# Kernel tuning notes

Hardware: AMD Instinct MI355X
Metric: run time of the kernel (lower is better)

The kernel has to match this reference:

```python
import jax, jax.numpy as jnp
import numpy as np

EPS = 1e-5
K_NN = 16

def _lin1d(x, W, b):
    # 1x1 Conv1d: x (B,C,N) -> (B,O,N)
    return jnp.einsum('oc,bcn->bon', W, x) + b[None, :, None]

def _lin2d(x, W, b):
    # 1x1 Conv2d: x (B,C,N,K) -> (B,O,N,K)
    return jnp.einsum('oc,bcnk->bonk', W, x) + b[None, :, None, None]

def _bn2d(x, gamma, beta):
    # train-mode BatchNorm2d over (B, N, K) per channel
    mean = jnp.mean(x, axis=(0, 2, 3), keepdims=True)
    var = jnp.var(x, axis=(0, 2, 3), keepdims=True)
    xh = (x - mean) * jax.lax.rsqrt(var + EPS)
    return gamma[None, :, None, None] * xh + beta[None, :, None, None]

def _knn_idx(pq, ps, k):
    # pq (B,3,N), ps (B,3,M) -> idx (B,N,K) of k nearest support points
    d2 = (jnp.sum(pq * pq, axis=1)[:, :, None]
          + jnp.sum(ps * ps, axis=1)[:, None, :]
          - 2.0 * jnp.einsum('bcn,bcm->bnm', pq, ps))
    _, idx = jax.lax.top_k(-d2, k)
    return idx

def _group(x, idx):
    # x (B,C,M), idx (B,N,K) -> (B,C,N,K)
    return jnp.take_along_axis(x[:, :, None, :], idx[:, None, :, :], axis=3)

def setup_inputs() -> dict:
    key = jax.random.key(0)
    ks = jax.random.split(key, 20)
    B, C, D, N, M, H = 4, 128, 64, 2048, 2048, 256
    s = lambda k, shape, scale: (jax.random.normal(k, shape, dtype=jnp.float32) * scale)
    return {
        'pq': s(ks[0], (B, 3, N), 1.0),
        'fq': s(ks[1], (B, C, N), 1.0),
        'ps': s(ks[2], (B, 3, M), 1.0),
        'fs': s(ks[3], (B, C, M), 1.0),
        'Wq': s(ks[4], (D, C), 0.05), 'bq': jnp.zeros((D,), jnp.float32),
        'Wk': s(ks[5], (D, C), 0.05), 'bk': jnp.zeros((D,), jnp.float32),
        'Wv': s(ks[6], (D, C), 0.05), 'bv': jnp.zeros((D,), jnp.float32),
        'Wp1': s(ks[7], (D, 3), 0.2), 'bp1': jnp.zeros((D,), jnp.float32),
        'gp': jnp.ones((D,), jnp.float32), 'btp': jnp.zeros((D,), jnp.float32),
        'Wp2': s(ks[8], (D, D), 0.05), 'bp2': jnp.zeros((D,), jnp.float32),
        'Wa1': s(ks[9], (H, D), 0.05), 'ba1': jnp.zeros((H,), jnp.float32),
        'ga': jnp.ones((H,), jnp.float32), 'bta': jnp.zeros((H,), jnp.float32),
        'Wa2': s(ks[10], (D, H), 0.05), 'ba2': jnp.zeros((D,), jnp.float32),
        'We': s(ks[11], (C, D), 0.05), 'be': jnp.zeros((C,), jnp.float32),
    }

def reference(pq, fq, ps, fs, Wq, bq, Wk, bk, Wv, bv,
              Wp1, bp1, gp, btp, Wp2, bp2,
              Wa1, ba1, ga, bta, Wa2, ba2, We, be):
    identity = fq
    q = _lin1d(fq, Wq, bq)          # (B,D,N)
    k = _lin1d(fs, Wk, bk)          # (B,D,M)
    v = _lin1d(fs, Wv, bv)          # (B,D,M)
    idx = _knn_idx(pq, ps, K_NN)    # (B,N,K)
    key_g = _group(k, idx)          # (B,D,N,K)
    qk_rel = q[:, :, :, None] - key_g
    pos_rel = pq[:, :, :, None] - _group(ps, idx)  # (B,3,N,K)
    # pos_mlp: conv-bn-relu-conv
    pe = _lin2d(pos_rel, Wp1, bp1)
    pe = jax.nn.relu(_bn2d(pe, gp, btp))
    pe = _lin2d(pe, Wp2, bp2)       # (B,D,N,K)
    # attn_mlp: conv-bn-relu-conv
    a = _lin2d(qk_rel + pe, Wa1, ba1)
    a = jax.nn.relu(_bn2d(a, ga, bta))
    a = _lin2d(a, Wa2, ba2)         # (B,D,N,K)
    attn = jax.nn.softmax(a, axis=-1)
    val = _group(v, idx) + pe       # (B,D,N,K)
    agg = jnp.einsum('bcnk,bcnk->bcn', attn, val)
    return _lin1d(agg, We, be) + identity
```

## Files before the change

kernel.cpp:

```cpp
#include <hip/hip_runtime.h>
#include <stdint.h>

#define NN 2048
#define MM 2048
#define NSAMP 131072

typedef float  fv4 __attribute__((ext_vector_type(4)));
typedef short  bfv8 __attribute__((ext_vector_type(8)));
typedef short  bfv4 __attribute__((ext_vector_type(4)));
typedef unsigned short u16;
typedef unsigned long long u64;

__device__ inline u16 f2bf(float x){
  unsigned u = __float_as_uint(x);
  return (u16)((u + 0x7FFFu + ((u>>16)&1u)) >> 16);
}
__device__ inline float bf2f(u16 u){ return __uint_as_float(((unsigned)u)<<16); }
#define MFMA16 __builtin_amdgcn_mfma_f32_16x16x32_bf16

__global__ __launch_bounds__(256) void k_front(
    const float* __restrict__ pq, const float* __restrict__ ps,
    const float* __restrict__ fq, const float* __restrict__ fs,
    const float* __restrict__ Wq, const float* __restrict__ Wk, const float* __restrict__ Wv,
    const float* __restrict__ Wp2, const float* __restrict__ Wa2, const float* __restrict__ We,
    const float* __restrict__ bq, const float* __restrict__ bk, const float* __restrict__ bv,
    u16* __restrict__ Wp2bf, u16* __restrict__ Wa2bf, u16* __restrict__ Webf,
    float* __restrict__ qT, float* __restrict__ kT, float* __restrict__ vT,
    int* __restrict__ idxb, float* __restrict__ posPart) {
  __shared__ __align__(16) unsigned char smem[35072];
  const int bid = blockIdx.x;
  const int t = threadIdx.x;

  if (bid < 64) {
    int gid = bid * 256 + t;
    if (gid < 4096)  Wp2bf[gid] = f2bf(Wp2[gid]);
    if (gid < 16384) Wa2bf[gid] = f2bf(Wa2[gid]);
    if (gid < 8192)  Webf[gid]  = f2bf(We[gid]);
    return;
  }

  if (bid < 320) {
    u16* tile0 = (u16*)smem;
    u16* tile1 = (u16*)(smem + 8704);
    int r = bid - 64;
    int b = r >> 6, p0 = (r & 63) * 32;
    int w = t >> 6, l = t & 63, lq = l >> 4, ln = l & 15;
    {
      int cq = t >> 3, n4 = (t & 7) * 4;
      #pragma unroll
      for (int it = 0; it < 4; ++it) {
        int c = it * 32 + cq;
        fv4 vq = *(const fv4*)&fq[(b*128 + c)*2048 + p0 + n4];
        fv4 vs = *(const fv4*)&fs[(b*128 + c)*2048 + p0 + n4];
        #pragma unroll
        for (int j = 0; j < 4; ++j) {
          tile0[(n4 + j)*136 + c] = f2bf(vq[j]);
          tile1[(n4 + j)*136 + c] = f2bf(vs[j]);
        }
      }
    }
    bfv8 A[3][4];
    #pragma unroll
    for (int mat = 0; mat < 3; ++mat) {
      const float* Wf = mat == 0 ? Wq : (mat == 1 ? Wk : Wv);
      #pragma unroll
      for (int kk = 0; kk < 4; ++kk) {
        const float* src = Wf + (w*16 + ln)*128 + kk*32 + lq*8;
        fv4 a0 = *(const fv4*)src, a1 = *(const fv4*)(src + 4);
        u16 tmp[8];
        #pragma unroll
        for (int e = 0; e < 4; ++e) { tmp[e] = f2bf(a0[e]); tmp[4+e] = f2bf(a1[e]); }
        A[mat][kk] = *(const bfv8*)tmp;
      }
    }
    __syncthreads();
    fv4 acc[3][2];
    #pragma unroll
    for (int mat = 0; mat < 3; ++mat) {
      const u16* tl = mat == 0 ? tile0 : tile1;
      #pragma unroll
      for (int nt = 0; nt < 2; ++nt) {
        fv4 a = {0.f,0.f,0.f,0.f};
        #pragma unroll
        for (int kk = 0; kk < 4; ++kk) {
          bfv8 bb = *(const bfv8*)&tl[(nt*16 + ln)*136 + kk*32 + lq*8];
          a = MFMA16(A[mat][kk], bb, a, 0, 0, 0);
        }
        acc[mat][nt] = a;
      }
    }
    #pragma unroll
    for (int mat = 0; mat < 3; ++mat) {
      float* dst = mat == 0 ? qT : (mat == 1 ? kT : vT);
      const float* bia = mat == 0 ? bq : (mat == 1 ? bk : bv);
      fv4 bq4 = *(const fv4*)&bia[w*16 + lq*4];
      #pragma unroll
      for (int nt = 0; nt < 2; ++nt) {
        fv4 o = acc[mat][nt] + bq4;
        *(fv4*)&dst[(b*NN + p0 + nt*16 + ln)*64 + w*16 + lq*4] = o;
      }
    }
    return;
  }

  {
    u64*   cand = (u64*)smem;
    float* sacc = (float*)(smem + 34816);
    int w = t >> 6, lane = t & 63;
    int blk = bid - 320;
    int qi = blk * 4 + w;
    int b = qi >> 11, n = qi & 2047;
    const float* pqb = pq + b * 3 * NN;
    const float* psb = ps + b * 3 * MM;
    float qx = pqb[n], qy = pqb[NN + n], qz = pqb[2 * NN + n];
    float qq = qx * qx + qy * qy + qz * qz;

    u64 A[16], Bv[16];
    #pragma unroll
    for (int j = 0; j < 16; ++j) {
      int m = lane + 64 * j;
      float sx = psb[m], sy = psb[MM + m], sz = psb[2 * MM + m];
      float ss  = sx * sx + sy * sy + sz * sz;
      float d2 = qq + ss - 2.f * (qx * sx + qy * sy + qz * sz);
      unsigned bu = __float_as_uint(d2);
      bu = (bu & 0x80000000u) ? ~bu : (bu | 0x80000000u);
      A[j] = (((u64)bu) << 32) | (unsigned)m;
    }
    #pragma unroll
    for (int j = 0; j < 16; ++j) {
      int m = lane + 64 * (j + 16);
      float sx = psb[m], sy = psb[MM + m], sz = psb[2 * MM + m];
      float ss  = sx * sx + sy * sy + sz * sz;
      float d2 = qq + ss - 2.f * (qx * sx + qy * sy + qz * sz);
      unsigned bu = __float_as_uint(d2);
      bu = (bu & 0x80000000u) ? ~bu : (bu | 0x80000000u);
      Bv[j] = (((u64)bu) << 32) | (unsigned)m;
    }
    #pragma unroll
    for (int k = 2; k <= 16; k <<= 1) {
      #pragma unroll
      for (int j = k >> 1; j > 0; j >>= 1) {
        #pragma unroll
        for (int i = 0; i < 16; ++i) {
          int l2 = i ^ j;
          if (l2 > i) {
            bool up = ((i & k) == 0);
            { u64 x = A[i], y = A[l2];
              bool sw = up ? (y < x) : (x < y);
              A[i] = sw ? y : x;  A[l2] = sw ? x : y; }
            { u64 x = Bv[i], y = Bv[l2];
              bool sw = up ? (y < x) : (x < y);
              Bv[i] = sw ? y : x; Bv[l2] = sw ? x : y; }
          }
        }
      }
    }
    #pragma unroll
    for (int i = 0; i < 16; ++i) {
      u64 y = Bv[15 - i];
      A[i] = A[i] < y ? A[i] : y;
    }
    #pragma unroll
    for (int j = 8; j > 0; j >>= 1) {
      #pragma unroll
      for (int i = 0; i < 16; ++i) {
        int l2 = i ^ j;
        if (l2 > i) {
          u64 x = A[i], y = A[l2];
          bool sw = (y < x);
          A[i] = sw ? y : x;  A[l2] = sw ? x : y;
        }
      }
    }
    #pragma unroll
    for (int i = 0; i < 16; ++i) cand[w*1088 + lane*17 + i] = A[i];
    float s0=0.f,s1=0.f,s2=0.f,s3=0.f,s4=0.f,s5=0.f,s6=0.f,s7=0.f,s8=0.f;
    int head = 0;
    for (int r = 0; r < 16; ++r) {
      u64 v = (head < 16) ? cand[w*1088 + lane*17 + head] : ~0ULL;
      u64 mv = v;
      #pragma unroll
      for (int off = 32; off > 0; off >>= 1) {
        u64 o = __shfl_xor(mv, off, 64);
        mv = o < mv ? o : mv;
      }
      if (v == mv) head++;
      unsigned m = (unsigned)(mv & 0xFFFFFFFFu);
      if (lane == 0) idxb[qi * 16 + r] = (int)m;
      float r0 = qx - psb[m], r1 = qy - psb[MM + m], r2 = qz - psb[2*MM + m];
      s0 += r0; s1 += r1; s2 += r2;
      s3 += r0*r0; s4 += r0*r1; s5 += r0*r2;
      s6 += r1*r1; s7 += r1*r2; s8 += r2*r2;
    }
    if (lane == 0) {
      sacc[w*9+0]=s0; sacc[w*9+1]=s1; sacc[w*9+2]=s2; sacc[w*9+3]=s3; sacc[w*9+4]=s4;
      sacc[w*9+5]=s5; sacc[w*9+6]=s6; sacc[w*9+7]=s7; sacc[w*9+8]=s8;
    }
    __syncthreads();
    if (t < 9) posPart[blk * 12 + t] =
        sacc[t] + sacc[9 + t] + sacc[18 + t] + sacc[27 + t];
  }
}

__global__ __launch_bounds__(256) void k_posfinal(
    const float* __restrict__ Wp1, const float* __restrict__ bp1,
    const float* __restrict__ gp, const float* __restrict__ btp,
    const float* __restrict__ posPart, float* __restrict__ Wp1f, float* __restrict__ bp1f) {
  __shared__ float red[4][9];
  __shared__ float st[9];
  int t = threadIdx.x;
  int w = t >> 6, lane = t & 63;
  float s[9];
  #pragma unroll
  for (int i = 0; i < 9; ++i) s[i] = 0.f;
  #pragma unroll
  for (int it = 0; it < 8; ++it) {
    const float* p = posPart + (it * 256 + t) * 12;
    fv4 a = *(const fv4*)p;
    fv4 b4 = *(const fv4*)(p + 4);
    float c8 = p[8];
    s[0]+=a.x; s[1]+=a.y; s[2]+=a.z; s[3]+=a.w;
    s[4]+=b4.x; s[5]+=b4.y; s[6]+=b4.z; s[7]+=b4.w;
    s[8]+=c8;
  }
  #pragma unroll
  for (int off = 32; off > 0; off >>= 1)
    #pragma unroll
    for (int i = 0; i < 9; ++i) s[i] += __shfl_xor(s[i], off, 64);
  if (lane == 0)
    #pragma unroll
    for (int i = 0; i < 9; ++i) red[w][i] = s[i];
  __syncthreads();
  if (t < 9) st[t] = red[0][t] + red[1][t] + red[2][t] + red[3][t];
  __syncthreads();
  if (t < 64) {
    int d = t;
    const float invN = 1.f / (float)NSAMP;
    float m0 = st[0]*invN, m1 = st[1]*invN, m2 = st[2]*invN;
    float C00 = st[3]*invN - m0*m0, C01 = st[4]*invN - m0*m1, C02 = st[5]*invN - m0*m2;
    float C11 = st[6]*invN - m1*m1, C12 = st[7]*invN - m1*m2, C22 = st[8]*invN - m2*m2;
    float w0 = Wp1[d*3], w1 = Wp1[d*3+1], w2 = Wp1[d*3+2];
    float mean = w0*m0 + w1*m1 + w2*m2 + bp1[d];
    float var = w0*w0*C00 + w1*w1*C11 + w2*w2*C22 + 2.f*(w0*w1*C01 + w0*w2*C02 + w1*w2*C12);
    float scale = gp[d] * rsqrtf(var + 1e-5f);
    Wp1f[d*3]   = scale * w0;
    Wp1f[d*3+1] = scale * w1;
    Wp1f[d*3+2] = scale * w2;
    bp1f[d] = btp[d] + scale * (bp1[d] - mean);
  }
}

__global__ __launch_bounds__(256) void k_ystats(
    const float* __restrict__ pq, const float* __restrict__ ps,
    const float* __restrict__ qT, const float* __restrict__ kT,
    const int* __restrict__ idxb,
    const float* __restrict__ Wp1f, const float* __restrict__ bp1f,
    const u16* __restrict__ Wp2bf, const float* __restrict__ bp2,
    float* __restrict__ Gpart, float* __restrict__ ySumPart) {
  __shared__ __align__(16) unsigned char smem[21760];
  u16*   hp   = (u16*)smem;
  u16*   y2   = (u16*)(smem + 9216);
  float* r3   = (float*)(smem + 18432);
  float* qc   = (float*)(smem + 19200);
  int*   idxA = (int*)(smem + 20224);
  float* sWp1 = (float*)(smem + 20480);
  float* sbp1 = (float*)(smem + 21248);
  float* sbp2 = (float*)(smem + 21504);

  const int t = threadIdx.x;
  const int w = t >> 6, l = t & 63, lq = l >> 4, ln = l & 15;
  const int d0 = 16*w + lq*4;

  if (t < 192) sWp1[t] = Wp1f[t];
  if (t < 64){ sbp1[t] = bp1f[t]; sbp2[t] = bp2[t]; }

  bfv8 Ape[2];
  #pragma unroll
  for (int kk = 0; kk < 2; ++kk)
    Ape[kk] = *(const bfv8*)(Wp2bf + (16*w + ln)*64 + kk*32 + lq*8);

  fv4 gacc[4];
  #pragma unroll
  for (int nt = 0; nt < 4; ++nt) gacc[nt] = (fv4){0.f,0.f,0.f,0.f};
  float ys[4] = {0.f, 0.f, 0.f, 0.f};
  __syncthreads();

  for (int ch = 0; ch < 4; ++ch) {
    const int p0 = blockIdx.x * 16 + ch * 4;
    const int b  = p0 >> 11;
    const int bN = b * 2048;
    if (t < 64) idxA[t] = idxb[p0*16 + t];
    qc[t] = qT[(p0 + (t>>6))*64 + (t & 63)];
    __syncthreads();
    if (t < 192) { int c = t >> 6, s = t & 63; int n = (p0 + (s>>4)) & 2047;
      r3[c*64 + s] = pq[(b*3+c)*NN + n] - ps[(b*3+c)*MM + idxA[s]]; }
    __syncthreads();
    { int s = t >> 2, iq = t & 3;
      float r0 = r3[s], r1 = r3[64+s], r2 = r3[128+s];
      u16 tmp[16];
      #pragma unroll
      for (int e = 0; e < 16; ++e) { int i = iq*16 + e;
        float v = sbp1[i] + sWp1[i*3]*r0 + sWp1[i*3+1]*r1 + sWp1[i*3+2]*r2;
        tmp[e] = f2bf(fmaxf(v, 0.f)); }
      *(bfv8*)&hp[s*72 + iq*16]     = *(const bfv8*)&tmp[0];
      *(bfv8*)&hp[s*72 + iq*16 + 8] = *(const bfv8*)&tmp[8];
    }
    __syncthreads();
    {
      fv4 pe[4];
      #pragma unroll
      for (int nt = 0; nt < 4; ++nt) {
        fv4 acc = {0.f,0.f,0.f,0.f};
        #pragma unroll
        for (int kk = 0; kk < 2; ++kk) {
          bfv8 bb = *(const bfv8*)&hp[(nt*16 + ln)*72 + kk*32 + lq*8];
          acc = MFMA16(Ape[kk], bb, acc, 0, 0, 0);
        }
        pe[nt] = acc;
      }
      fv4 bp2q = *(const fv4*)&sbp2[d0];
      #pragma unroll
      for (int nt = 0; nt < 4; ++nt) {
        int s = nt*16 + ln;
        int mi = idxA[s];
        fv4 kg = *(const fv4*)(kT + (bN + mi)*64 + d0);
        fv4 qv = *(const fv4*)&qc[nt*64 + d0];
        fv4 yv = qv - kg + pe[nt] + bp2q;
        #pragma unroll
        for (int r = 0; r < 4; ++r) { y2[(d0 + r)*72 + s] = f2bf(yv[r]); ys[r] += yv[r]; }
      }
    }
    __syncthreads();
    #pragma unroll
    for (int kk = 0; kk < 2; ++kk) {
      bfv8 aa = *(const bfv8*)&y2[(16*w + ln)*72 + kk*32 + lq*8];
      #pragma unroll
      for (int nt = 0; nt < 4; ++nt) {
        bfv8 bb = *(const bfv8*)&y2[(nt*16 + ln)*72 + kk*32 + lq*8];
        gacc[nt] = MFMA16(aa, bb, gacc[nt], 0, 0, 0);
      }
    }
    __syncthreads();
  }
  #pragma unroll
  for (int nt = 0; nt < 4; ++nt)
    #pragma unroll
    for (int r = 0; r < 4; ++r)
      Gpart[blockIdx.x*4096 + (16*w + lq*4 + r)*64 + nt*16 + ln] = gacc[nt][r];
  #pragma unroll
  for (int off = 1; off <= 8; off <<= 1) {
    #pragma unroll
    for (int r = 0; r < 4; ++r) ys[r] += __shfl_xor(ys[r], off, 64);
  }
  if (ln == 0) {
    #pragma unroll
    for (int r = 0; r < 4; ++r) ySumPart[blockIdx.x*64 + d0 + r] = ys[r];
  }
}

__global__ __launch_bounds__(256) void k_gred(
    const float* __restrict__ Gpart, const float* __restrict__ ySumPart,
    float* __restrict__ G, float* __restrict__ ySum) {
  int bid = blockIdx.x, t = threadIdx.x;
  if (bid < 16) {
    int j = bid*256 + t;
    float s = 0.f;
    for (int p = 0; p < 512; ++p) s += Gpart[p*4096 + j];
    G[j] = s;
  } else if (t < 64) {
    float s = 0.f;
    for (int p = 0; p < 512; ++p) s += ySumPart[p*64 + t];
    ySum[t] = s;
  }
}

__global__ __launch_bounds__(256) void k_attnfinal(
    const float* __restrict__ Wa1, const float* __restrict__ ba1,
    const float* __restrict__ ga, const float* __restrict__ bta,
    const float* __restrict__ ySum, const float* __restrict__ G,
    u16* __restrict__ Wa1fbf, float* __restrict__ ba1f) {
  __shared__ float red[256];
  __shared__ float mu[64];
  __shared__ float sc[1];
  int h = blockIdx.x, t = threadIdx.x;
  const float invN = 1.f / (float)NSAMP;
  if (t < 64) mu[t] = ySum[t] * invN;
  __syncthreads();
  float acc = 0.f;
  #pragma unroll
  for (int e = 0; e < 16; ++e) {
    int pi = t*16 + e, i = pi >> 6, j = pi & 63;
    float cov = G[pi]*invN - mu[i]*mu[j];
    acc += Wa1[h*64 + i] * Wa1[h*64 + j] * cov;
  }
  red[t] = acc;
  __syncthreads();
  for (int s = 128; s > 0; s >>= 1) { if (t < s) red[t] += red[t + s]; __syncthreads(); }
  float var = red[0];
  __syncthreads();
  red[t] = (t < 64) ? Wa1[h*64 + t] * mu[t] : 0.f;
  __syncthreads();
  for (int s = 128; s > 0; s >>= 1) { if (t < s) red[t] += red[t + s]; __syncthreads(); }
  if (t == 0) {
    float mean  = red[0] + ba1[h];
    float scale = ga[h] * rsqrtf(var + 1e-5f);
    sc[0] = scale;
    ba1f[h] = bta[h] + scale * (ba1[h] - mean);
  }
  __syncthreads();
  if (t < 64) Wa1fbf[h*64 + t] = f2bf(sc[0] * Wa1[h*64 + t]);
}

__global__ __launch_bounds__(256) void k_main(
    const float* __restrict__ pq, const float* __restrict__ ps,
    const float* __restrict__ qT, const float* __restrict__ kT, const float* __restrict__ vT,
    const int* __restrict__ idxb,
    const float* __restrict__ Wp1f, const float* __restrict__ bp1f,
    const u16* __restrict__ Wp2bf, const float* __restrict__ bp2,
    const u16* __restrict__ Wa1fbf, const float* __restrict__ ba1f,
    const u16* __restrict__ Wa2bf, const float* __restrict__ ba2,
    const u16* __restrict__ Webf, const float* __restrict__ be,
    const float* __restrict__ fq,
    u16* __restrict__ aggbf, float* __restrict__ out) {
  __shared__ __align__(16) unsigned char smem[65024];
  u16*   hp   = (u16*)smem;
  u16*   ha   = (u16*)smem;
  u16*   ylds = (u16*)(smem + 33792);
  float* at   = (float*)(smem + 33792);
  u16*   vt   = (u16*)(smem + 51200);
  float* r3   = (float*)(smem + 60416);
  float* qc   = (float*)(smem + 61184);
  int*   idxA = (int*)(smem + 62208);
  float* sWp1 = (float*)(smem + 62464);
  float* sbp1 = (float*)(smem + 63232);
  float* sbp2 = (float*)(smem + 63488);
  float* sba1 = (float*)(smem + 63744);
  float* sba2 = (float*)(smem + 64768);

  const int t = threadIdx.x;
  const int w = t >> 6, l = t & 63, lq = l >> 4, ln = l & 15;
  const int d0 = 16*w + lq*4;

  if (t < 192) sWp1[t] = Wp1f[t];
  if (t < 64){ sbp1[t] = bp1f[t]; sbp2[t] = bp2[t]; sba2[t] = ba2[t]; }
  sba1[t] = ba1f[t];

  bfv8 Ape[2], A1[4][2], A2[8];
  #pragma unroll
  for (int kk = 0; kk < 2; ++kk)
    Ape[kk] = *(const bfv8*)(Wp2bf + (16*w + ln)*64 + kk*32 + lq*8);
  #pragma unroll
  for (int mt = 0; mt < 4; ++mt)
    #pragma unroll
    for (int kk = 0; kk < 2; ++kk)
      A1[mt][kk] = *(const bfv8*)(Wa1fbf + (64*w + mt*16 + ln)*64 + kk*32 + lq*8);
  #pragma unroll
  for (int kk = 0; kk < 8; ++kk)
    A2[kk] = *(const bfv8*)(Wa2bf + (16*w + ln)*256 + kk*32 + lq*8);
  __syncthreads();

  for (int ch = 0; ch < 4; ++ch) {
    const int p0 = blockIdx.x * 16 + ch * 4;
    const int b  = p0 >> 11;
    const int bN = b * 2048;
    if (t < 64) idxA[t] = idxb[p0*16 + t];
    qc[t] = qT[(p0 + (t>>6))*64 + (t & 63)];
    __syncthreads();
    if (t < 192) { int c = t >> 6, s = t & 63; int n = (p0 + (s>>4)) & 2047;
      r3[c*64 + s] = pq[(b*3+c)*NN + n] - ps[(b*3+c)*MM + idxA[s]]; }
    __syncthreads();
    { int s = t >> 2, iq = t & 3;
      float r0 = r3[s], r1 = r3[64+s], r2 = r3[128+s];
      u16 tmp[16];
      #pragma unroll
      for (int e = 0; e < 16; ++e) { int i = iq*16 + e;
        float v = sbp1[i] + sWp1[i*3]*r0 + sWp1[i*3+1]*r1 + sWp1[i*3+2]*r2;
        tmp[e] = f2bf(fmaxf(v, 0.f)); }
      *(bfv8*)&hp[s*72 + iq*16]     = *(const bfv8*)&tmp[0];
      *(bfv8*)&hp[s*72 + iq*16 + 8] = *(const bfv8*)&tmp[8];
    }
    __syncthreads();
    {
      fv4 pe[4];
      #pragma unroll
      for (int nt = 0; nt < 4; ++nt) {
        fv4 acc = {0.f,0.f,0.f,0.f};
        #pragma unroll
        for (int kk = 0; kk < 2; ++kk) {
          bfv8 bb = *(const bfv8*)&hp[(nt*16 + ln)*72 + kk*32 + lq*8];
          acc = MFMA16(Ape[kk], bb, acc, 0, 0, 0);
        }
        pe[nt] = acc;
      }
      fv4 bp2q = *(const fv4*)&sbp2[d0];
      #pragma unroll
      for (int nt = 0; nt < 4; ++nt) {
        int s = nt*16 + ln;
        int mi = idxA[s];
        fv4 kg = *(const fv4*)(kT + (bN + mi)*64 + d0);
        fv4 vg = *(const fv4*)(vT + (bN + mi)*64 + d0);
        fv4 qv = *(const fv4*)&qc[nt*64 + d0];
        fv4 pv = pe[nt] + bp2q;
        fv4 yv = qv - kg + pv;
        fv4 vv = vg + pv;
        u16 yp[4], vp[4];
        #pragma unroll
        for (int r = 0; r < 4; ++r) { yp[r] = f2bf(yv[r]); vp[r] = f2bf(vv[r]); }
        *(bfv4*)&ylds[s*72 + d0] = *(const bfv4*)yp;
        *(bfv4*)&vt[s*72 + d0]   = *(const bfv4*)vp;
      }
    }
    __syncthreads();
    #pragma unroll
    for (int nt = 0; nt < 4; ++nt) {
      int s = nt*16 + ln;
      bfv8 b0 = *(const bfv8*)&ylds[s*72 + lq*8];
      bfv8 b1 = *(const bfv8*)&ylds[s*72 + 32 + lq*8];
      #pragma unroll
      for (int mt = 0; mt < 4; ++mt) {
        fv4 acc = {0.f,0.f,0.f,0.f};
        acc = MFMA16(A1[mt][0], b0, acc, 0, 0, 0);
        acc = MFMA16(A1[mt][1], b1, acc, 0, 0, 0);
        int h0 = 64*w + mt*16 + lq*4;
        fv4 bq = *(const fv4*)&sba1[h0];
        u16 hv[4];
        #pragma unroll
        for (int r = 0; r < 4; ++r) hv[r] = f2bf(fmaxf(acc[r] + bq[r], 0.f));
        *(bfv4*)&ha[s*264 + h0] = *(const bfv4*)hv;
      }
    }
    __syncthreads();
    {
      fv4 acc2[4];
      #pragma unroll
      for (int nt = 0; nt < 4; ++nt) acc2[nt] = (fv4){0.f,0.f,0.f,0.f};
      #pragma unroll
      for (int kk = 0; kk < 8; ++kk) {
        #pragma unroll
        for (int nt = 0; nt < 4; ++nt) {
          bfv8 bb = *(const bfv8*)&ha[(nt*16 + ln)*264 + kk*32 + lq*8];
          acc2[nt] = MFMA16(A2[kk], bb, acc2[nt], 0, 0, 0);
        }
      }
      fv4 ba2q = *(const fv4*)&sba2[d0];
      #pragma unroll
      for (int nt = 0; nt < 4; ++nt) {
        int s = nt*16 + ln;
        fv4 o = acc2[nt] + ba2q;
        *(fv4*)&at[s*68 + d0] = o;
      }
    }
    __syncthreads();
    {
      int dd = t & 63, pt = t >> 6;
      float a[16];
      #pragma unroll
      for (int k = 0; k < 16; ++k) a[k] = at[(pt*16 + k)*68 + dd];
      float mx = a[0];
      #pragma unroll
      for (int k = 1; k < 16; ++k) mx = fmaxf(mx, a[k]);
      float sum = 0.f, num = 0.f;
      #pragma unroll
      for (int k = 0; k < 16; ++k) {
        float e = __expf(a[k] - mx);
        sum += e;
        num += e * bf2f(vt[(pt*16 + k)*72 + dd]);
      }
      aggbf[(p0 + pt)*64 + dd] = f2bf(num / sum);
    }
    __syncthreads();
  }
  {
    const int P0 = blockIdx.x * 16;
    const int b  = P0 >> 11;
    const int n0 = P0 & 2047;
    bfv8 EA[2][2];
    #pragma unroll
    for (int mt = 0; mt < 2; ++mt)
      #pragma unroll
      for (int kk = 0; kk < 2; ++kk)
        EA[mt][kk] = *(const bfv8*)(Webf + ((w*2 + mt)*16 + ln)*64 + kk*32 + lq*8);
    const u16* bp = aggbf + (P0 + ln)*64;
    bfv8 b0 = *(const bfv8*)(bp + lq*8);
    bfv8 b1 = *(const bfv8*)(bp + 32 + lq*8);
    fv4 eacc[2];
    #pragma unroll
    for (int mt = 0; mt < 2; ++mt) {
      fv4 a = {0.f,0.f,0.f,0.f};
      a = MFMA16(EA[mt][0], b0, a, 0, 0, 0);
      a = MFMA16(EA[mt][1], b1, a, 0, 0, 0);
      eacc[mt] = a;
    }
    #pragma unroll
    for (int mt = 0; mt < 2; ++mt) {
      int c0 = (w*2 + mt)*16 + lq*4;
      fv4 bev = *(const fv4*)&be[c0];
      #pragma unroll
      for (int r = 0; r < 4; ++r) {
        int c = c0 + r;
        int o = (b*128 + c)*2048 + n0 + ln;
        out[o] = eacc[mt][r] + bev[r] + fq[o];
      }
    }
  }
}

extern "C" void kernel_launch(void* const* d_in, const int* in_sizes, int n_in,
                              void* d_out, int out_size, void* d_ws, size_t ws_size,
                              hipStream_t stream) {
  (void)in_sizes; (void)n_in; (void)out_size; (void)ws_size;
  const float* pq  = (const float*)d_in[0];
  const float* fq  = (const float*)d_in[1];
  const float* ps  = (const float*)d_in[2];
  const float* fs  = (const float*)d_in[3];
  const float* Wq  = (const float*)d_in[4];  const float* bq  = (const float*)d_in[5];
  const float* Wk  = (const float*)d_in[6];  const float* bk  = (const float*)d_in[7];
  const float* Wv  = (const float*)d_in[8];  const float* bv  = (const float*)d_in[9];
  const float* Wp1 = (const float*)d_in[10]; const float* bp1 = (const float*)d_in[11];
  const float* gp  = (const float*)d_in[12]; const float* btp = (const float*)d_in[13];
  const float* Wp2 = (const float*)d_in[14]; const float* bp2 = (const float*)d_in[15];
  const float* Wa1 = (const float*)d_in[16]; const float* ba1 = (const float*)d_in[17];
  const float* ga  = (const float*)d_in[18]; const float* bta = (const float*)d_in[19];
  const float* Wa2 = (const float*)d_in[20]; const float* ba2 = (const float*)d_in[21];
  const float* We  = (const float*)d_in[22]; const float* be  = (const float*)d_in[23];
  float* ws = (float*)d_ws;
  float* qT    = ws;
  float* kT    = ws + 524288;
  float* vT    = ws + 1048576;
  u16*   aggbf = (u16*)(ws + 1572864);
  int*   idxb  = (int*)(ws + 2097152);
  float* Wp1f  = ws + 2375680;
  float* bp1f  = ws + 2375872;
  float* ba1f  = ws + 2375936;
  float* G     = ws + 2376192;
  float* ySum  = ws + 2380288;
  float* ySumP = ws + 2380352;
  u16*   Wp2bf  = (u16*)(ws + 2413120);
  u16*   Wa2bf  = (u16*)(ws + 2415168);
  u16*   Wa1fbf = (u16*)(ws + 2423360);
  u16*   Webf   = (u16*)(ws + 2431552);
  float* posPart = ws + 2435648;
  float* Gpart   = ws + 2460224;
  float* out   = (float*)d_out;

  k_front<<<2368, 256, 0, stream>>>(pq, ps, fq, fs, Wq, Wk, Wv, Wp2, Wa2, We,
                                    bq, bk, bv, Wp2bf, Wa2bf, Webf,
                                    qT, kT, vT, idxb, posPart);
  k_posfinal<<<1, 256, 0, stream>>>(Wp1, bp1, gp, btp, posPart, Wp1f, bp1f);
  k_ystats<<<512, 256, 0, stream>>>(pq, ps, qT, kT, idxb, Wp1f, bp1f, Wp2bf, bp2,
                                    Gpart, ySumP);
  k_gred<<<17, 256, 0, stream>>>(Gpart, ySumP, G, ySum);
  k_attnfinal<<<256, 256, 0, stream>>>(Wa1, ba1, ga, bta, ySum, G, Wa1fbf, ba1f);
  k_main<<<512, 256, 0, stream>>>(pq, ps, qT, kT, vT, idxb, Wp1f, bp1f, Wp2bf, bp2,
                                  Wa1fbf, ba1f, Wa2bf, ba2, Webf, be, fq, aggbf, out);
}
```

Before: 246.6 us.

## Fuse pos-BN finalize into ystats, halve per-block points, shuffle softmax in main

```diff
diff --git a/kernel.cpp b/kernel.cpp
--- a/kernel.cpp
+++ b/kernel.cpp
@@ -202,62 +202,17 @@
   }
 }
 
-__global__ __launch_bounds__(256) void k_posfinal(
-    const float* __restrict__ Wp1, const float* __restrict__ bp1,
-    const float* __restrict__ gp, const float* __restrict__ btp,
-    const float* __restrict__ posPart, float* __restrict__ Wp1f, float* __restrict__ bp1f) {
-  __shared__ float red[4][9];
-  __shared__ float st[9];
-  int t = threadIdx.x;
-  int w = t >> 6, lane = t & 63;
-  float s[9];
-  #pragma unroll
-  for (int i = 0; i < 9; ++i) s[i] = 0.f;
-  #pragma unroll
-  for (int it = 0; it < 8; ++it) {
-    const float* p = posPart + (it * 256 + t) * 12;
-    fv4 a = *(const fv4*)p;
-    fv4 b4 = *(const fv4*)(p + 4);
-    float c8 = p[8];
-    s[0]+=a.x; s[1]+=a.y; s[2]+=a.z; s[3]+=a.w;
-    s[4]+=b4.x; s[5]+=b4.y; s[6]+=b4.z; s[7]+=b4.w;
-    s[8]+=c8;
-  }
-  #pragma unroll
-  for (int off = 32; off > 0; off >>= 1)
-    #pragma unroll
-    for (int i = 0; i < 9; ++i) s[i] += __shfl_xor(s[i], off, 64);
-  if (lane == 0)
-    #pragma unroll
-    for (int i = 0; i < 9; ++i) red[w][i] = s[i];
-  __syncthreads();
-  if (t < 9) st[t] = red[0][t] + red[1][t] + red[2][t] + red[3][t];
-  __syncthreads();
-  if (t < 64) {
-    int d = t;
-    const float invN = 1.f / (float)NSAMP;
-    float m0 = st[0]*invN, m1 = st[1]*invN, m2 = st[2]*invN;
-    float C00 = st[3]*invN - m0*m0, C01 = st[4]*invN - m0*m1, C02 = st[5]*invN - m0*m2;
-    float C11 = st[6]*invN - m1*m1, C12 = st[7]*invN - m1*m2, C22 = st[8]*invN - m2*m2;
-    float w0 = Wp1[d*3], w1 = Wp1[d*3+1], w2 = Wp1[d*3+2];
-    float mean = w0*m0 + w1*m1 + w2*m2 + bp1[d];
-    float var = w0*w0*C00 + w1*w1*C11 + w2*w2*C22 + 2.f*(w0*w1*C01 + w0*w2*C02 + w1*w2*C12);
-    float scale = gp[d] * rsqrtf(var + 1e-5f);
-    Wp1f[d*3]   = scale * w0;
-    Wp1f[d*3+1] = scale * w1;
-    Wp1f[d*3+2] = scale * w2;
-    bp1f[d] = btp[d] + scale * (bp1[d] - mean);
-  }
-}
-
 __global__ __launch_bounds__(256) void k_ystats(
     const float* __restrict__ pq, const float* __restrict__ ps,
     const float* __restrict__ qT, const float* __restrict__ kT,
     const int* __restrict__ idxb,
-    const float* __restrict__ Wp1f, const float* __restrict__ bp1f,
+    const float* __restrict__ Wp1, const float* __restrict__ bp1,
+    const float* __restrict__ gp, const float* __restrict__ btp,
+    const float* __restrict__ posPart,
     const u16* __restrict__ Wp2bf, const float* __restrict__ bp2,
-    float* __restrict__ Gpart, float* __restrict__ ySumPart) {
-  __shared__ __align__(16) unsigned char smem[21760];
+    u16* __restrict__ Gpart16, float* __restrict__ ySumPart,
+    float* __restrict__ Wp1fG, float* __restrict__ bp1fG) {
+  __shared__ __align__(16) unsigned char smem[22144];
   u16*   hp   = (u16*)smem;
   u16*   y2   = (u16*)(smem + 9216);
   float* r3   = (float*)(smem + 18432);
@@ -266,14 +221,59 @@
   float* sWp1 = (float*)(smem + 20480);
   float* sbp1 = (float*)(smem + 21248);
   float* sbp2 = (float*)(smem + 21504);
+  float* redp = (float*)(smem + 21760);
 
   const int t = threadIdx.x;
   const int w = t >> 6, l = t & 63, lq = l >> 4, ln = l & 15;
   const int d0 = 16*w + lq*4;
 
-  if (t < 192) sWp1[t] = Wp1f[t];
-  if (t < 64){ sbp1[t] = bp1f[t]; sbp2[t] = bp2[t]; }
-
+  {
+    float s[9];
+    #pragma unroll
+    for (int i = 0; i < 9; ++i) s[i] = 0.f;
+    #pragma unroll
+    for (int it = 0; it < 8; ++it) {
+      const float* p = posPart + (it * 256 + t) * 12;
+      fv4 a = *(const fv4*)p;
+      fv4 b4 = *(const fv4*)(p + 4);
+      float c8 = p[8];
+      s[0]+=a.x; s[1]+=a.y; s[2]+=a.z; s[3]+=a.w;
+      s[4]+=b4.x; s[5]+=b4.y; s[6]+=b4.z; s[7]+=b4.w;
+      s[8]+=c8;
+    }
+    #pragma unroll
+    for (int off = 32; off > 0; off >>= 1)
+      #pragma unroll
+      for (int i = 0; i < 9; ++i) s[i] += __shfl_xor(s[i], off, 64);
+    if (l == 0)
+      #pragma unroll
+      for (int i = 0; i < 9; ++i) redp[w*9 + i] = s[i];
+    __syncthreads();
+    if (t < 9) redp[36 + t] = redp[t] + redp[9+t] + redp[18+t] + redp[27+t];
+    __syncthreads();
+    if (t < 64) {
+      const float* st = redp + 36;
+      int d = t;
+      const float invN = 1.f / (float)NSAMP;
+      float m0 = st[0]*invN, m1 = st[1]*invN, m2 = st[2]*invN;
+      float C00 = st[3]*invN - m0*m0, C01 = st[4]*invN - m0*m1, C02 = st[5]*invN - m0*m2;
+      float C11 = st[6]*invN - m1*m1, C12 = st[7]*invN - m1*m2, C22 = st[8]*invN - m2*m2;
+      float w0 = Wp1[d*3], w1 = Wp1[d*3+1], w2 = Wp1[d*3+2];
+      float mean = w0*m0 + w1*m1 + w2*m2 + bp1[d];
+      float var = w0*w0*C00 + w1*w1*C11 + w2*w2*C22 + 2.f*(w0*w1*C01 + w0*w2*C02 + w1*w2*C12);
+      float scale = gp[d] * rsqrtf(var + 1e-5f);
+      sWp1[d*3]   = scale * w0;
+      sWp1[d*3+1] = scale * w1;
+      sWp1[d*3+2] = scale * w2;
+      float bf = btp[d] + scale * (bp1[d] - mean);
+      sbp1[d] = bf;
+      sbp2[d] = bp2[d];
+      if (blockIdx.x == 0) {
+        Wp1fG[d*3] = sWp1[d*3]; Wp1fG[d*3+1] = sWp1[d*3+1]; Wp1fG[d*3+2] = sWp1[d*3+2];
+        bp1fG[d] = bf;
+      }
+    }
+  }
   bfv8 Ape[2];
   #pragma unroll
   for (int kk = 0; kk < 2; ++kk)
@@ -285,8 +285,8 @@
   float ys[4] = {0.f, 0.f, 0.f, 0.f};
   __syncthreads();
 
-  for (int ch = 0; ch < 4; ++ch) {
-    const int p0 = blockIdx.x * 16 + ch * 4;
+  for (int ch = 0; ch < 2; ++ch) {
+    const int p0 = blockIdx.x * 8 + ch * 4;
     const int b  = p0 >> 11;
     const int bN = b * 2048;
     if (t < 64) idxA[t] = idxb[p0*16 + t];
@@ -346,7 +346,7 @@
   for (int nt = 0; nt < 4; ++nt)
     #pragma unroll
     for (int r = 0; r < 4; ++r)
-      Gpart[blockIdx.x*4096 + (16*w + lq*4 + r)*64 + nt*16 + ln] = gacc[nt][r];
+      Gpart16[blockIdx.x*4096 + (16*w + lq*4 + r)*64 + nt*16 + ln] = f2bf(gacc[nt][r]);
   #pragma unroll
   for (int off = 1; off <= 8; off <<= 1) {
     #pragma unroll
@@ -359,18 +359,29 @@
 }
 
 __global__ __launch_bounds__(256) void k_gred(
-    const float* __restrict__ Gpart, const float* __restrict__ ySumPart,
+    const u16* __restrict__ Gpart16, const float* __restrict__ ySumPart,
     float* __restrict__ G, float* __restrict__ ySum) {
+  __shared__ float red[256];
   int bid = blockIdx.x, t = threadIdx.x;
-  if (bid < 16) {
-    int j = bid*256 + t;
+  if (bid < 256) {
+    int j0 = bid * 16, tj = t & 15, st = t >> 4;
     float s = 0.f;
-    for (int p = 0; p < 512; ++p) s += Gpart[p*4096 + j];
-    G[j] = s;
-  } else if (t < 64) {
-    float s = 0.f;
-    for (int p = 0; p < 512; ++p) s += ySumPart[p*64 + t];
-    ySum[t] = s;
+    for (int p = 0; p < 64; ++p)
+      s += bf2f(Gpart16[(st*64 + p)*4096 + j0 + tj]);
+    red[t] = s;
+    __syncthreads();
+    if (t < 16) {
+      float ss = 0.f;
+      #pragma unroll
+      for (int k = 0; k < 16; ++k) ss += red[k*16 + t];
+      G[j0 + t] = ss;
+    }
+  } else {
+    if (t < 64) {
+      float s = 0.f;
+      for (int p = 0; p < 1024; ++p) s += ySumPart[p*64 + t];
+      ySum[t] = s;
+    }
   }
 }
 
@@ -411,7 +422,7 @@
   if (t < 64) Wa1fbf[h*64 + t] = f2bf(sc[0] * Wa1[h*64 + t]);
 }
 
-__global__ __launch_bounds__(256) void k_main(
+__global__ __launch_bounds__(256, 3) void k_main(
     const float* __restrict__ pq, const float* __restrict__ ps,
     const float* __restrict__ qT, const float* __restrict__ kT, const float* __restrict__ vT,
     const int* __restrict__ idxb,
@@ -420,22 +431,20 @@
     const u16* __restrict__ Wa1fbf, const float* __restrict__ ba1f,
     const u16* __restrict__ Wa2bf, const float* __restrict__ ba2,
     const u16* __restrict__ Webf, const float* __restrict__ be,
-    const float* __restrict__ fq,
-    u16* __restrict__ aggbf, float* __restrict__ out) {
-  __shared__ __align__(16) unsigned char smem[65024];
+    const float* __restrict__ fq, float* __restrict__ out) {
+  __shared__ __align__(16) unsigned char smem[48896];
   u16*   hp   = (u16*)smem;
   u16*   ha   = (u16*)smem;
   u16*   ylds = (u16*)(smem + 33792);
-  float* at   = (float*)(smem + 33792);
-  u16*   vt   = (u16*)(smem + 51200);
-  float* r3   = (float*)(smem + 60416);
-  float* qc   = (float*)(smem + 61184);
-  int*   idxA = (int*)(smem + 62208);
-  float* sWp1 = (float*)(smem + 62464);
-  float* sbp1 = (float*)(smem + 63232);
-  float* sbp2 = (float*)(smem + 63488);
-  float* sba1 = (float*)(smem + 63744);
-  float* sba2 = (float*)(smem + 64768);
+  u16*   agg  = (u16*)(smem + 43008);
+  float* r3   = (float*)(smem + 44288);
+  float* qc   = (float*)(smem + 45056);
+  int*   idxA = (int*)(smem + 46080);
+  float* sWp1 = (float*)(smem + 46336);
+  float* sbp1 = (float*)(smem + 47104);
+  float* sbp2 = (float*)(smem + 47360);
+  float* sba1 = (float*)(smem + 47616);
+  float* sba2 = (float*)(smem + 48640);
 
   const int t = threadIdx.x;
   const int w = t >> 6, l = t & 63, lq = l >> 4, ln = l & 15;
@@ -459,8 +468,8 @@
     A2[kk] = *(const bfv8*)(Wa2bf + (16*w + ln)*256 + kk*32 + lq*8);
   __syncthreads();
 
-  for (int ch = 0; ch < 4; ++ch) {
-    const int p0 = blockIdx.x * 16 + ch * 4;
+  for (int ch = 0; ch < 2; ++ch) {
+    const int p0 = blockIdx.x * 8 + ch * 4;
     const int b  = p0 >> 11;
     const int bN = b * 2048;
     if (t < 64) idxA[t] = idxb[p0*16 + t];
@@ -480,6 +489,7 @@
       *(bfv8*)&hp[s*72 + iq*16 + 8] = *(const bfv8*)&tmp[8];
     }
     __syncthreads();
+    fv4 vvr[4];
     {
       fv4 pe[4];
       #pragma unroll
@@ -502,12 +512,11 @@
         fv4 qv = *(const fv4*)&qc[nt*64 + d0];
         fv4 pv = pe[nt] + bp2q;
         fv4 yv = qv - kg + pv;
-        fv4 vv = vg + pv;
-        u16 yp[4], vp[4];
-        #pragma unroll
-        for (int r = 0; r < 4; ++r) { yp[r] = f2bf(yv[r]); vp[r] = f2bf(vv[r]); }
+        vvr[nt] = vg + pv;
+        u16 yp[4];
+        #pragma unroll
+        for (int r = 0; r < 4; ++r) yp[r] = f2bf(yv[r]);
         *(bfv4*)&ylds[s*72 + d0] = *(const bfv4*)yp;
-        *(bfv4*)&vt[s*72 + d0]   = *(const bfv4*)vp;
       }
     }
     __syncthreads();
@@ -545,33 +554,31 @@
       fv4 ba2q = *(const fv4*)&sba2[d0];
       #pragma unroll
       for (int nt = 0; nt < 4; ++nt) {
-        int s = nt*16 + ln;
-        fv4 o = acc2[nt] + ba2q;
-        *(fv4*)&at[s*68 + d0] = o;
-      }
-    }
-    __syncthreads();
-    {
-      int dd = t & 63, pt = t >> 6;
-      float a[16];
-      #pragma unroll
-      for (int k = 0; k < 16; ++k) a[k] = at[(pt*16 + k)*68 + dd];
-      float mx = a[0];
-      #pragma unroll
-      for (int k = 1; k < 16; ++k) mx = fmaxf(mx, a[k]);
-      float sum = 0.f, num = 0.f;
-      #pragma unroll
-      for (int k = 0; k < 16; ++k) {
-        float e = __expf(a[k] - mx);
-        sum += e;
-        num += e * bf2f(vt[(pt*16 + k)*72 + dd]);
-      }
-      aggbf[(p0 + pt)*64 + dd] = f2bf(num / sum);
+        fv4 a4 = acc2[nt] + ba2q;
+        u16 o4[4];
+        #pragma unroll
+        for (int r = 0; r < 4; ++r) {
+          float m = a4[r];
+          m = fmaxf(m, __shfl_xor(m, 1, 64));
+          m = fmaxf(m, __shfl_xor(m, 2, 64));
+          m = fmaxf(m, __shfl_xor(m, 4, 64));
+          m = fmaxf(m, __shfl_xor(m, 8, 64));
+          float e = __expf(a4[r] - m);
+          float se = e;
+          se += __shfl_xor(se, 1, 64); se += __shfl_xor(se, 2, 64);
+          se += __shfl_xor(se, 4, 64); se += __shfl_xor(se, 8, 64);
+          float nu = e * vvr[nt][r];
+          nu += __shfl_xor(nu, 1, 64); nu += __shfl_xor(nu, 2, 64);
+          nu += __shfl_xor(nu, 4, 64); nu += __shfl_xor(nu, 8, 64);
+          o4[r] = f2bf(nu / se);
+        }
+        if (ln == 0) *(bfv4*)&agg[(ch*4 + nt)*72 + d0] = *(const bfv4*)o4;
+      }
     }
     __syncthreads();
   }
   {
-    const int P0 = blockIdx.x * 16;
+    const int P0 = blockIdx.x * 8;
     const int b  = P0 >> 11;
     const int n0 = P0 & 2047;
     bfv8 EA[2][2];
@@ -580,9 +587,11 @@
       #pragma unroll
       for (int kk = 0; kk < 2; ++kk)
         EA[mt][kk] = *(const bfv8*)(Webf + ((w*2 + mt)*16 + ln)*64 + kk*32 + lq*8);
-    const u16* bp = aggbf + (P0 + ln)*64;
-    bfv8 b0 = *(const bfv8*)(bp + lq*8);
-    bfv8 b1 = *(const bfv8*)(bp + 32 + lq*8);
+    bfv8 b0 = {0,0,0,0,0,0,0,0}, b1 = {0,0,0,0,0,0,0,0};
+    if (ln < 8) {
+      b0 = *(const bfv8*)&agg[ln*72 + lq*8];
+      b1 = *(const bfv8*)&agg[ln*72 + 32 + lq*8];
+    }
     fv4 eacc[2];
     #pragma unroll
     for (int mt = 0; mt < 2; ++mt) {
@@ -591,15 +600,17 @@
       a = MFMA16(EA[mt][1], b1, a, 0, 0, 0);
       eacc[mt] = a;
     }
-    #pragma unroll
-    for (int mt = 0; mt < 2; ++mt) {
-      int c0 = (w*2 + mt)*16 + lq*4;
-      fv4 bev = *(const fv4*)&be[c0];
-      #pragma unroll
-      for (int r = 0; r < 4; ++r) {
-        int c = c0 + r;
-        int o = (b*128 + c)*2048 + n0 + ln;
-        out[o] = eacc[mt][r] + bev[r] + fq[o];
+    if (ln < 8) {
+      #pragma unroll
+      for (int mt = 0; mt < 2; ++mt) {
+        int c0 = (w*2 + mt)*16 + lq*4;
+        fv4 bev = *(const fv4*)&be[c0];
+        #pragma unroll
+        for (int r = 0; r < 4; ++r) {
+          int c = c0 + r;
+          int o = (b*128 + c)*2048 + n0 + ln;
+          out[o] = eacc[mt][r] + bev[r] + fq[o];
+        }
       }
     }
   }
@@ -624,33 +635,32 @@
   const float* Wa2 = (const float*)d_in[20]; const float* ba2 = (const float*)d_in[21];
   const float* We  = (const float*)d_in[22]; const float* be  = (const float*)d_in[23];
   float* ws = (float*)d_ws;
-  float* qT    = ws;
-  float* kT    = ws + 524288;
-  float* vT    = ws + 1048576;
-  u16*   aggbf = (u16*)(ws + 1572864);
-  int*   idxb  = (int*)(ws + 2097152);
-  float* Wp1f  = ws + 2375680;
-  float* bp1f  = ws + 2375872;
-  float* ba1f  = ws + 2375936;
-  float* G     = ws + 2376192;
-  float* ySum  = ws + 2380288;
-  float* ySumP = ws + 2380352;
-  u16*   Wp2bf  = (u16*)(ws + 2413120);
-  u16*   Wa2bf  = (u16*)(ws + 2415168);
-  u16*   Wa1fbf = (u16*)(ws + 2423360);
-  u16*   Webf   = (u16*)(ws + 2431552);
-  float* posPart = ws + 2435648;
-  float* Gpart   = ws + 2460224;
-  float* out   = (float*)d_out;
+  float* qT      = ws;
+  float* kT      = ws + 524288;
+  float* vT      = ws + 1048576;
+  int*   idxb    = (int*)(ws + 1572864);
+  float* Wp1f    = ws + 1703936;
+  float* bp1f    = ws + 1704128;
+  float* ba1f    = ws + 1704192;
+  float* G       = ws + 1704448;
+  float* ySum    = ws + 1708544;
+  float* ySumP   = ws + 1708608;
+  u16*   Wp2bf   = (u16*)(ws + 1774144);
+  u16*   Wa2bf   = (u16*)(ws + 1776192);
+  u16*   Wa1fbf  = (u16*)(ws + 1784384);
+  u16*   Webf    = (u16*)(ws + 1792576);
+  float* posPart = ws + 1796672;
+  u16*   Gpart16 = (u16*)(ws + 1821248);
+  float* out     = (float*)d_out;
 
   k_front<<<2368, 256, 0, stream>>>(pq, ps, fq, fs, Wq, Wk, Wv, Wp2, Wa2, We,
                                     bq, bk, bv, Wp2bf, Wa2bf, Webf,
                                     qT, kT, vT, idxb, posPart);
-  k_posfinal<<<1, 256, 0, stream>>>(Wp1, bp1, gp, btp, posPart, Wp1f, bp1f);
-  k_ystats<<<512, 256, 0, stream>>>(pq, ps, qT, kT, idxb, Wp1f, bp1f, Wp2bf, bp2,
-                                    Gpart, ySumP);
-  k_gred<<<17, 256, 0, stream>>>(Gpart, ySumP, G, ySum);
+  k_ystats<<<1024, 256, 0, stream>>>(pq, ps, qT, kT, idxb,
+                                     Wp1, bp1, gp, btp, posPart, Wp2bf, bp2,
+                                     Gpart16, ySumP, Wp1f, bp1f);
+  k_gred<<<257, 256, 0, stream>>>(Gpart16, ySumP, G, ySum);
   k_attnfinal<<<256, 256, 0, stream>>>(Wa1, ba1, ga, bta, ySum, G, Wa1fbf, ba1f);
-  k_main<<<512, 256, 0, stream>>>(pq, ps, qT, kT, vT, idxb, Wp1f, bp1f, Wp2bf, bp2,
-                                  Wa1fbf, ba1f, Wa2bf, ba2, Webf, be, fq, aggbf, out);
+  k_main<<<1024, 256, 0, stream>>>(pq, ps, qT, kT, vT, idxb, Wp1f, bp1f, Wp2bf, bp2,
+                                   Wa1fbf, ba1f, Wa2bf, ba2, Webf, be, fq, out);
 }
```

After: 268.7 us. 9.0% more time.
